# Optimization experiments

Hardware: AMD Instinct MI355X
Metric: run time of the kernel (lower is better)

## Reference

```python
import jax, jax.numpy as jnp
import numpy as np

DIM = 2048
N_HEADS = 16
N_KV_HEADS = 4
HEAD_DIM = 128
EPS = 1e-6
BS, SEQ = 2, 4096


def setup_inputs() -> dict:
    key = jax.random.key(0)
    ks = jax.random.split(key, 8)
    x = jax.random.normal(ks[0], (BS, SEQ, DIM), dtype=jnp.float32)
    # rotary freqs: unit-modulus complex represented as [seq, head_dim//2, 2]
    theta = 10000.0
    inv_freq = 1.0 / (theta ** (jnp.arange(0, HEAD_DIM, 2, dtype=jnp.float32) / HEAD_DIM))
    t = jnp.arange(SEQ, dtype=jnp.float32)
    ang = jnp.outer(t, inv_freq)  # [SEQ, HEAD_DIM//2]
    freqs_cis = jnp.stack([jnp.cos(ang), jnp.sin(ang)], axis=-1)  # [SEQ, HD/2, 2]
    std = 0.02
    wq = jax.random.normal(ks[1], (N_HEADS * HEAD_DIM, DIM), dtype=jnp.float32) * std
    wk = jax.random.normal(ks[2], (N_KV_HEADS * HEAD_DIM, DIM), dtype=jnp.float32) * std
    wv = jax.random.normal(ks[3], (N_KV_HEADS * HEAD_DIM, DIM), dtype=jnp.float32) * std
    wo = jax.random.normal(ks[4], (DIM, N_HEADS * HEAD_DIM), dtype=jnp.float32) * std
    q_norm_w = jnp.ones((HEAD_DIM,), dtype=jnp.float32)
    k_norm_w = jnp.ones((HEAD_DIM,), dtype=jnp.float32)
    return {"x": x, "freqs_cis": freqs_cis, "wq": wq, "wk": wk, "wv": wv,
            "wo": wo, "q_norm_w": q_norm_w, "k_norm_w": k_norm_w}


def _rms_norm(x, w, eps=EPS):
    xf = x.astype(jnp.float32)
    var = jnp.mean(xf * xf, axis=-1, keepdims=True)
    return w * (xf * jax.lax.rsqrt(var + eps)).astype(x.dtype)


def _apply_rope(x, freqs_cis):
    # x: [b, s, h, d]; freqs_cis: [s, d//2, 2] (cos, sin)
    b, s, h, d = x.shape
    xr = x.astype(jnp.float32).reshape(b, s, h, d // 2, 2)
    cos = freqs_cis[:s, :, 0][None, :, None, :]
    sin = freqs_cis[:s, :, 1][None, :, None, :]
    xre, xim = xr[..., 0], xr[..., 1]
    out = jnp.stack([xre * cos - xim * sin, xre * sin + xim * cos], axis=-1)
    return out.reshape(b, s, h, d).astype(x.dtype)


def reference(x, freqs_cis, wq, wk, wv, wo, q_norm_w, k_norm_w):
    bs, seqlen, _ = x.shape
    xq = jnp.einsum('bsd,ed->bse', x, wq).reshape(bs, seqlen, N_HEADS, HEAD_DIM)
    xk = jnp.einsum('bsd,ed->bse', x, wk).reshape(bs, seqlen, N_KV_HEADS, HEAD_DIM)
    xv = jnp.einsum('bsd,ed->bse', x, wv).reshape(bs, seqlen, N_KV_HEADS, HEAD_DIM)
    xq = _rms_norm(xq, q_norm_w)
    xk = _rms_norm(xk, k_norm_w)
    xq = _apply_rope(xq, freqs_cis)
    xk = _apply_rope(xk, freqs_cis)
    n_rep = N_HEADS // N_KV_HEADS
    # repeat_kv: [b,s,kvh,d] -> [b,s,kvh*n_rep,d]
    keys = jnp.repeat(xk, n_rep, axis=2)
    values = jnp.repeat(xv, n_rep, axis=2)
    q = xq.transpose(0, 2, 1, 3)  # [b,h,s,d]
    k = keys.transpose(0, 2, 1, 3)
    v = values.transpose(0, 2, 1, 3)
    scale = 1.0 / jnp.sqrt(jnp.asarray(HEAD_DIM, dtype=q.dtype))
    scores = jnp.einsum('bhqd,bhkd->bhqk', q, k) * scale
    causal = jnp.tril(jnp.ones((seqlen, seqlen), dtype=bool))
    scores = jnp.where(causal[None, None], scores, jnp.finfo(scores.dtype).min)
    attn = jax.nn.softmax(scores, axis=-1)
    out = jnp.einsum('bhqk,bhkd->bhqd', attn, v)
    out = out.transpose(0, 2, 1, 3).reshape(bs, seqlen, N_HEADS * HEAD_DIM)
    return jnp.einsum('bse,de->bsd', out, wo)
```

## Files before the change

kernel.cpp:

```cpp
#include <hip/hip_runtime.h>

typedef __bf16 bf16;
typedef __bf16 bf16x8 __attribute__((ext_vector_type(8)));
typedef __bf16 bf16x4 __attribute__((ext_vector_type(4)));
typedef __bf16 bf16x2 __attribute__((ext_vector_type(2)));
typedef float  f32x4  __attribute__((ext_vector_type(4)));

static_assert(sizeof(bf16x8) == 16, "bf16x8 must be 16B");

#define MFMA16(a, b, c) __builtin_amdgcn_mfma_f32_16x16x32_bf16((a), (b), (c), 0, 0, 0)

__device__ __forceinline__ void gload_lds16(const void* g, void* l) {
    __builtin_amdgcn_global_load_lds(
        (const __attribute__((address_space(1))) void*)(uintptr_t)g,
        (__attribute__((address_space(3))) void*)(uintptr_t)l,
        16, 0, 0);
}

__global__ __launch_bounds__(256)
void cast_f32_bf16(const float* __restrict__ in, bf16* __restrict__ out, int n8)
{
    const int i = blockIdx.x * 256 + threadIdx.x;
    if (i >= n8) return;
    const float4 a = ((const float4*)in)[i * 2];
    const float4 b = ((const float4*)in)[i * 2 + 1];
    bf16x8 o;
    o[0] = (bf16)a.x; o[1] = (bf16)a.y; o[2] = (bf16)a.z; o[3] = (bf16)a.w;
    o[4] = (bf16)b.x; o[5] = (bf16)b.y; o[6] = (bf16)b.z; o[7] = (bf16)b.w;
    ((bf16x8*)out)[i] = o;
}

template <typename OT>
__global__ __launch_bounds__(256)
void gemm_bt(const bf16* __restrict__ A, const bf16* __restrict__ W,
             int K, int ldc, OT* __restrict__ C)
{
    __shared__ bf16 As[128 * 32];
    __shared__ bf16 Bs[128 * 32];

    const int n0 = blockIdx.x * 128;
    const int m0 = blockIdx.y * 128;

    const int tid  = threadIdx.x;
    const int lane = tid & 63;
    const int wid  = tid >> 6;
    const int wm   = wid >> 1;
    const int wn   = wid & 1;
    const int quad = lane >> 4;
    const int l16  = lane & 15;

    const int srow = wid * 32 + (lane >> 2);
    const int scol = (lane & 3) * 8;
    const bf16* ag = A + (size_t)(m0 + srow) * K + scol;
    const bf16* wg = W + (size_t)(n0 + srow) * K + scol;
    bf16* al = As + wid * 1024;
    bf16* bl = Bs + wid * 1024;

    const bf16* afr = As + (wm * 64 + l16) * 32 + quad * 8;
    const bf16* bfr = Bs + (wn * 64 + l16) * 32 + quad * 8;

    f32x4 acc[4][4];
#pragma unroll
    for (int i = 0; i < 4; i++)
#pragma unroll
        for (int j = 0; j < 4; j++) acc[i][j] = f32x4{0.f, 0.f, 0.f, 0.f};

    for (int kt = 0; kt < K; kt += 32) {
        __syncthreads();
        gload_lds16(ag,          al);
        gload_lds16(ag + 16 * K, al + 512);
        gload_lds16(wg,          bl);
        gload_lds16(wg + 16 * K, bl + 512);
        ag += 32; wg += 32;
        __syncthreads();

        bf16x8 af[4], bfv[4];
#pragma unroll
        for (int i = 0; i < 4; i++) af[i]  = *(const bf16x8*)(afr + i * 16 * 32);
#pragma unroll
        for (int i = 0; i < 4; i++) bfv[i] = *(const bf16x8*)(bfr + i * 16 * 32);
#pragma unroll
        for (int mi = 0; mi < 4; mi++)
#pragma unroll
            for (int ni = 0; ni < 4; ni++)
                acc[mi][ni] = MFMA16(af[mi], bfv[ni], acc[mi][ni]);
    }

#pragma unroll
    for (int mi = 0; mi < 4; mi++) {
        const int row = m0 + wm * 64 + mi * 16 + quad * 4;
#pragma unroll
        for (int ni = 0; ni < 4; ni++) {
            const int col = n0 + wn * 64 + ni * 16 + l16;
#pragma unroll
            for (int r = 0; r < 4; r++)
                C[(size_t)(row + r) * ldc + col] = (OT)acc[mi][ni][r];
        }
    }
}

__global__ __launch_bounds__(256)
void normrope(bf16* __restrict__ qkv, const float* __restrict__ fc,
              const float* __restrict__ qw, const float* __restrict__ kw)
{
    const int row  = blockIdx.x * 4 + (threadIdx.x >> 6);
    const int lane = threadIdx.x & 63;
    const int slot = row % 20;
    const int tok  = row / 20;
    const int s    = tok & 4095;

    const float* w; int off; float post;
    if (slot < 16) { off = slot * 128;               w = qw; post = 0.12751681555f; }
    else           { off = 2048 + (slot - 16) * 128; w = kw; post = 1.0f; }

    bf16* p = qkv + (size_t)tok * 3072 + off;

    bf16x2 v = *(const bf16x2*)(p + 2 * lane);
    float x0 = (float)v[0], x1 = (float)v[1];

    float ss = x0 * x0 + x1 * x1;
    ss += __shfl_xor(ss, 1);  ss += __shfl_xor(ss, 2);  ss += __shfl_xor(ss, 4);
    ss += __shfl_xor(ss, 8);  ss += __shfl_xor(ss, 16); ss += __shfl_xor(ss, 32);
    const float r = rsqrtf(ss * (1.0f / 128.0f) + 1e-6f) * post;

    const float xn0 = x0 * r * w[2 * lane], xn1 = x1 * r * w[2 * lane + 1];

    const float2 cs = ((const float2*)fc)[(size_t)s * 64 + lane];
    const float c = cs.x, sn = cs.y;

    bf16x2 o;
    o[0] = (bf16)(xn0 * c - xn1 * sn);
    o[1] = (bf16)(xn0 * sn + xn1 * c);
    *(bf16x2*)(p + 2 * lane) = o;
}

__global__ __launch_bounds__(256)
void transpose_v(const bf16* __restrict__ qkv, bf16* __restrict__ vT)
{
    const int idx = blockIdx.x;
    const int d   = idx & 127;
    const int bk  = idx >> 7;
    const int b   = bk >> 2;
    const int kvh = bk & 3;
    const bf16* src = qkv + (size_t)b * 4096 * 3072 + 2560 + kvh * 128 + d;
    bf16* dst = vT + (size_t)idx * 4096;
    for (int s = threadIdx.x; s < 4096; s += 256)
        dst[s] = src[(size_t)s * 3072];
}

__global__ __launch_bounds__(256)
void flash(const bf16* __restrict__ qkv, const bf16* __restrict__ vT,
           bf16* __restrict__ out)
{
    const int bh  = blockIdx.y;
    const int b   = bh >> 4, h = bh & 15;
    const int kvh = h >> 2;

    const int tid  = threadIdx.x;
    const int lane = tid & 63;
    const int wid  = tid >> 6;
    const int quad = lane >> 4;
    const int l16  = lane & 15;
    const int key  = l16 & 7;

    __shared__ bf16 Ks[2][64 * 128];
    __shared__ bf16 Vs[128 * 64];
    __shared__ bf16 Ps[128 * 64];

    const bf16* kbase = qkv + (size_t)b * 4096 * 3072 + 2048 + kvh * 128;
    const bf16* vbase = vT + ((size_t)(b * 4 + kvh) * 128) * 4096;

    const int krow_off = lane >> 4;
    const int kcolg    = lane & 15;
    const int vrow_off = lane >> 3;
    const int vcolg    = lane & 7;

    for (int pass = 0; pass < 2; ++pass) {
        const int qt = pass ? (31 - blockIdx.x) : blockIdx.x;
        const int q0 = qt * 128;
        const int ntiles = qt * 2 + 2;

        __syncthreads();
#pragma unroll
        for (int i = 0; i < 4; i++) {
            const int r0 = wid * 16 + i * 4;
            const int rk = r0 + krow_off;
            const int gc = (kcolg ^ (rk & 7)) * 8;
            gload_lds16(kbase + (size_t)rk * 3072 + gc, &Ks[0][r0 * 128]);
        }

        bf16x8 qf[2][4];
        const bf16* qbase = qkv + ((size_t)(b * 4096 + q0 + wid * 32)) * 3072 + h * 128;
#pragma unroll
        for (int mt = 0; mt < 2; mt++)
#pragma unroll
            for (int ks = 0; ks < 4; ks++)
                qf[mt][ks] = *(const bf16x8*)(qbase + (size_t)(mt * 16 + l16) * 3072 + ks * 32 + quad * 8);

        f32x4 oacc[2][8];
#pragma unroll
        for (int mt = 0; mt < 2; mt++)
#pragma unroll
            for (int nd = 0; nd < 8; nd++) oacc[mt][nd] = f32x4{0.f, 0.f, 0.f, 0.f};
        float mrow[2], lrow[2];
#pragma unroll
        for (int mt = 0; mt < 2; mt++) { mrow[mt] = -__builtin_inff(); lrow[mt] = 0.f; }

        int cur = 0;
        for (int t = 0; t < ntiles; t++) {
            const int kv0 = t * 64;
            __syncthreads();

#pragma unroll
            for (int i = 0; i < 4; i++) {
                const int r0 = wid * 32 + i * 8;
                const int dv = r0 + vrow_off;
                const int gc = (vcolg ^ (dv & 7)) * 8;
                gload_lds16(vbase + (size_t)dv * 4096 + kv0 + gc, &Vs[r0 * 64]);
            }
            const int kvn = (t + 1 < ntiles) ? kv0 + 64 : kv0;
#pragma unroll
            for (int i = 0; i < 4; i++) {
                const int r0 = wid * 16 + i * 4;
                const int rk = r0 + krow_off;
                const int gc = (kcolg ^ (rk & 7)) * 8;
                gload_lds16(kbase + (size_t)(kvn + rk) * 3072 + gc, &Ks[1 - cur][r0 * 128]);
            }

            f32x4 sacc[2][4];
#pragma unroll
            for (int mt = 0; mt < 2; mt++)
#pragma unroll
                for (int nt = 0; nt < 4; nt++) sacc[mt][nt] = f32x4{0.f, 0.f, 0.f, 0.f};
            __builtin_amdgcn_s_setprio(1);
#pragma unroll
            for (int ks = 0; ks < 4; ks++) {
                bf16x8 kf[4];
#pragma unroll
                for (int nt = 0; nt < 4; nt++)
                    kf[nt] = *(const bf16x8*)(&Ks[cur][(nt * 16 + l16) * 128 + (((ks * 4 + quad) ^ key) * 8)]);
#pragma unroll
                for (int mt = 0; mt < 2; mt++)
#pragma unroll
                    for (int nt = 0; nt < 4; nt++)
                        sacc[mt][nt] = MFMA16(kf[nt], qf[mt][ks], sacc[mt][nt]);
            }
            __builtin_amdgcn_s_setprio(0);

            if (kv0 + 63 > q0) {
#pragma unroll
                for (int mt = 0; mt < 2; mt++) {
                    const int qg = q0 + wid * 32 + mt * 16 + l16;
#pragma unroll
                    for (int nt = 0; nt < 4; nt++)
#pragma unroll
                        for (int r = 0; r < 4; r++) {
                            const int kvg = kv0 + nt * 16 + quad * 4 + r;
                            if (kvg > qg) sacc[mt][nt][r] = -1e30f;
                        }
                }
            }

            float pm[2];
#pragma unroll
            for (int mt = 0; mt < 2; mt++) {
                float t8[8];
#pragma unroll
                for (int nt = 0; nt < 4; nt++) {
                    t8[2 * nt]     = fmaxf(sacc[mt][nt][0], sacc[mt][nt][1]);
                    t8[2 * nt + 1] = fmaxf(sacc[mt][nt][2], sacc[mt][nt][3]);
                }
                float m = fmaxf(fmaxf(fmaxf(t8[0], t8[1]), fmaxf(t8[2], t8[3])),
                                fmaxf(fmaxf(t8[4], t8[5]), fmaxf(t8[6], t8[7])));
                m = fmaxf(m, __shfl_xor(m, 16));
                m = fmaxf(m, __shfl_xor(m, 32));
                pm[mt] = m;
            }

            const bool rescale =
                !__all((pm[0] - mrow[0] <= 8.f) && (pm[1] - mrow[1] <= 8.f));
            if (rescale) {
#pragma unroll
                for (int mt = 0; mt < 2; mt++) {
                    const float mnew  = fmaxf(mrow[mt], pm[mt]);
                    const float alpha = exp2f(mrow[mt] - mnew);
                    mrow[mt] = mnew;
                    lrow[mt] *= alpha;
                    float ar[4];
#pragma unroll
                    for (int r = 0; r < 4; r++) ar[r] = __shfl(alpha, quad * 4 + r);
#pragma unroll
                    for (int nd = 0; nd < 8; nd++)
#pragma unroll
                        for (int r = 0; r < 4; r++) oacc[mt][nd][r] *= ar[r];
                }
            }

#pragma unroll
            for (int mt = 0; mt < 2; mt++) {
                const int prow = wid * 32 + mt * 16 + l16;
                float sn[4];
#pragma unroll
                for (int nt = 0; nt < 4; nt++) {
                    const float p0 = exp2f(sacc[mt][nt][0] - mrow[mt]);
                    const float p1 = exp2f(sacc[mt][nt][1] - mrow[mt]);
                    const float p2 = exp2f(sacc[mt][nt][2] - mrow[mt]);
                    const float p3 = exp2f(sacc[mt][nt][3] - mrow[mt]);
                    sn[nt] = (p0 + p1) + (p2 + p3);
                    bf16x4 h4;
                    h4[0] = (bf16)p0; h4[1] = (bf16)p1;
                    h4[2] = (bf16)p2; h4[3] = (bf16)p3;
                    const int g = (2 * nt + (quad >> 1)) ^ key;
                    *(bf16x4*)(&Ps[prow * 64 + g * 8 + (quad & 1) * 4]) = h4;
                }
                float s = (sn[0] + sn[1]) + (sn[2] + sn[3]);
                s += __shfl_xor(s, 16);
                s += __shfl_xor(s, 32);
                lrow[mt] += s;
            }

            __syncthreads();

            __builtin_amdgcn_s_setprio(1);
#pragma unroll
            for (int ks = 0; ks < 2; ks++) {
                bf16x8 pf[2];
#pragma unroll
                for (int mt = 0; mt < 2; mt++)
                    pf[mt] = *(const bf16x8*)(&Ps[(wid * 32 + mt * 16 + l16) * 64 + (((ks * 4 + quad) ^ key) * 8)]);
#pragma unroll
                for (int nd = 0; nd < 8; nd++) {
                    const bf16x8 vf = *(const bf16x8*)(&Vs[(nd * 16 + l16) * 64 + (((ks * 4 + quad) ^ key) * 8)]);
#pragma unroll
                    for (int mt = 0; mt < 2; mt++)
                        oacc[mt][nd] = MFMA16(pf[mt], vf, oacc[mt][nd]);
                }
            }
            __builtin_amdgcn_s_setprio(0);
            cur ^= 1;
        }

#pragma unroll
        for (int mt = 0; mt < 2; mt++) {
            const float inv = 1.0f / lrow[mt];
            float invr[4];
#pragma unroll
            for (int r = 0; r < 4; r++) invr[r] = __shfl(inv, quad * 4 + r);
#pragma unroll
            for (int r = 0; r < 4; r++) {
                const size_t srow = (size_t)(b * 4096 + q0 + wid * 32 + mt * 16 + quad * 4 + r);
#pragma unroll
                for (int nd = 0; nd < 8; nd++)
                    out[srow * 2048 + h * 128 + nd * 16 + l16] = (bf16)(oacc[mt][nd][r] * invr[r]);
            }
        }
    }
}

extern "C" void kernel_launch(void* const* d_in, const int* in_sizes, int n_in,
                              void* d_out, int out_size, void* d_ws, size_t ws_size,
                              hipStream_t stream)
{
    const float* x   = (const float*)d_in[0];
    const float* fc  = (const float*)d_in[1];
    const float* wq  = (const float*)d_in[2];
    const float* wk  = (const float*)d_in[3];
    const float* wv  = (const float*)d_in[4];
    const float* wo  = (const float*)d_in[5];
    const float* qnw = (const float*)d_in[6];
    const float* knw = (const float*)d_in[7];
    float* out = (float*)d_out;

    char* ws = (char*)d_ws;
    bf16* qkv = (bf16*)ws;
    bf16* vT  = (bf16*)(ws + 50331648);
    bf16* xb  = (bf16*)(ws + 58720256);
    bf16* att = xb;
    bf16* wb  = (bf16*)(ws + 92274688);
    bf16* wob = wb;

    cast_f32_bf16<<<dim3(8192), 256, 0, stream>>>(x, xb, 2097152);
    cast_f32_bf16<<<dim3(2048), 256, 0, stream>>>(wq, wb, 524288);
    cast_f32_bf16<<<dim3(512),  256, 0, stream>>>(wk, wb + 2048 * 2048, 131072);
    cast_f32_bf16<<<dim3(512),  256, 0, stream>>>(wv, wb + 2560 * 2048, 131072);
    gemm_bt<bf16><<<dim3(24, 64), 256, 0, stream>>>(xb, wb, 2048, 3072, qkv);
    normrope<<<dim3(40960), 256, 0, stream>>>(qkv, fc, qnw, knw);
    transpose_v<<<dim3(1024), 256, 0, stream>>>(qkv, vT);
    flash<<<dim3(16, 32), 256, 0, stream>>>(qkv, vT, att);
    cast_f32_bf16<<<dim3(2048), 256, 0, stream>>>(wo, wob, 524288);
    gemm_bt<float><<<dim3(16, 64), 256, 0, stream>>>(att, wob, 2048, 2048, out);
}
```

Before: 696.9 us.

## Compute softmax row sums via MFMA with ones, tile V transpose through LDS

The flash kernel now accumulates the softmax denominator by running an extra MFMA of the bf16 P fragments against a vector of ones. This replaces the per-tile exp-sum adds and cross-lane shuffles, and the sum now uses the bf16-rounded P, which matches the numerator. The V transpose kernel moves from strided scalar loads to 64x128 tiles staged through shared memory, giving coalesced reads and writes. The redundant K prefetch on the last tile is also skipped. The cost is extra MFMA work and slightly different rounding in the normaliser.

```diff
diff --git a/kernel.cpp b/kernel.cpp
--- a/kernel.cpp
+++ b/kernel.cpp
@@ -137,15 +137,32 @@
 __global__ __launch_bounds__(256)
 void transpose_v(const bf16* __restrict__ qkv, bf16* __restrict__ vT)
 {
-    const int idx = blockIdx.x;
-    const int d   = idx & 127;
-    const int bk  = idx >> 7;
-    const int b   = bk >> 2;
-    const int kvh = bk & 3;
-    const bf16* src = qkv + (size_t)b * 4096 * 3072 + 2560 + kvh * 128 + d;
-    bf16* dst = vT + (size_t)idx * 4096;
-    for (int s = threadIdx.x; s < 4096; s += 256)
-        dst[s] = src[(size_t)s * 3072];
+    __shared__ bf16 T[64][130];
+    const int st = blockIdx.x;
+    const int bk = blockIdx.y;
+    const int b = bk >> 2, kvh = bk & 3;
+    const int w = threadIdx.x >> 6, lane = threadIdx.x & 63;
+    const int s0 = st * 64;
+
+    const bf16* src = qkv + (size_t)(b * 4096 + s0) * 3072 + 2560 + kvh * 128;
+#pragma unroll
+    for (int i = 0; i < 16; i++) {
+        const int s = w * 16 + i;
+        const bf16x2 v = *(const bf16x2*)(src + (size_t)s * 3072 + 2 * lane);
+        *(bf16x2*)(&T[s][2 * lane]) = v;
+    }
+    __syncthreads();
+
+    bf16* dst = vT + ((size_t)bk * 128) * 4096 + s0;
+#pragma unroll
+    for (int i = 0; i < 16; i++) {
+        const int d = w * 32 + 2 * i + (lane >> 5);
+        const int s = (lane & 31) * 2;
+        bf16x2 o;
+        o[0] = T[s][d];
+        o[1] = T[s + 1][d];
+        *(bf16x2*)(dst + (size_t)d * 4096 + s) = o;
+    }
 }
 
 __global__ __launch_bounds__(256)
@@ -175,6 +192,10 @@
     const int vrow_off = lane >> 3;
     const int vcolg    = lane & 7;
 
+    bf16x8 vone;
+#pragma unroll
+    for (int j = 0; j < 8; j++) vone[j] = (bf16)1.0f;
+
     for (int pass = 0; pass < 2; ++pass) {
         const int qt = pass ? (31 - blockIdx.x) : blockIdx.x;
         const int q0 = qt * 128;
@@ -198,13 +219,16 @@
                 qf[mt][ks] = *(const bf16x8*)(qbase + (size_t)(mt * 16 + l16) * 3072 + ks * 32 + quad * 8);
 
         f32x4 oacc[2][8];
-#pragma unroll
-        for (int mt = 0; mt < 2; mt++)
+        f32x4 lacc[2];
+#pragma unroll
+        for (int mt = 0; mt < 2; mt++) {
 #pragma unroll
             for (int nd = 0; nd < 8; nd++) oacc[mt][nd] = f32x4{0.f, 0.f, 0.f, 0.f};
-        float mrow[2], lrow[2];
-#pragma unroll
-        for (int mt = 0; mt < 2; mt++) { mrow[mt] = -__builtin_inff(); lrow[mt] = 0.f; }
+            lacc[mt] = f32x4{0.f, 0.f, 0.f, 0.f};
+        }
+        float mrow[2];
+#pragma unroll
+        for (int mt = 0; mt < 2; mt++) mrow[mt] = -__builtin_inff();
 
         int cur = 0;
         for (int t = 0; t < ntiles; t++) {
@@ -218,13 +242,15 @@
                 const int gc = (vcolg ^ (dv & 7)) * 8;
                 gload_lds16(vbase + (size_t)dv * 4096 + kv0 + gc, &Vs[r0 * 64]);
             }
-            const int kvn = (t + 1 < ntiles) ? kv0 + 64 : kv0;
-#pragma unroll
-            for (int i = 0; i < 4; i++) {
-                const int r0 = wid * 16 + i * 4;
-                const int rk = r0 + krow_off;
-                const int gc = (kcolg ^ (rk & 7)) * 8;
-                gload_lds16(kbase + (size_t)(kvn + rk) * 3072 + gc, &Ks[1 - cur][r0 * 128]);
+            if (t + 1 < ntiles) {
+                const int kvn = kv0 + 64;
+#pragma unroll
+                for (int i = 0; i < 4; i++) {
+                    const int r0 = wid * 16 + i * 4;
+                    const int rk = r0 + krow_off;
+                    const int gc = (kcolg ^ (rk & 7)) * 8;
+                    gload_lds16(kbase + (size_t)(kvn + rk) * 3072 + gc, &Ks[1 - cur][r0 * 128]);
+                }
             }
 
             f32x4 sacc[2][4];
@@ -285,7 +311,6 @@
                     const float mnew  = fmaxf(mrow[mt], pm[mt]);
                     const float alpha = exp2f(mrow[mt] - mnew);
                     mrow[mt] = mnew;
-                    lrow[mt] *= alpha;
                     float ar[4];
 #pragma unroll
                     for (int r = 0; r < 4; r++) ar[r] = __shfl(alpha, quad * 4 + r);
@@ -293,30 +318,26 @@
                     for (int nd = 0; nd < 8; nd++)
 #pragma unroll
                         for (int r = 0; r < 4; r++) oacc[mt][nd][r] *= ar[r];
+#pragma unroll
+                    for (int r = 0; r < 4; r++) lacc[mt][r] *= ar[r];
                 }
             }
 
 #pragma unroll
             for (int mt = 0; mt < 2; mt++) {
                 const int prow = wid * 32 + mt * 16 + l16;
-                float sn[4];
 #pragma unroll
                 for (int nt = 0; nt < 4; nt++) {
                     const float p0 = exp2f(sacc[mt][nt][0] - mrow[mt]);
                     const float p1 = exp2f(sacc[mt][nt][1] - mrow[mt]);
                     const float p2 = exp2f(sacc[mt][nt][2] - mrow[mt]);
                     const float p3 = exp2f(sacc[mt][nt][3] - mrow[mt]);
-                    sn[nt] = (p0 + p1) + (p2 + p3);
                     bf16x4 h4;
                     h4[0] = (bf16)p0; h4[1] = (bf16)p1;
                     h4[2] = (bf16)p2; h4[3] = (bf16)p3;
                     const int g = (2 * nt + (quad >> 1)) ^ key;
                     *(bf16x4*)(&Ps[prow * 64 + g * 8 + (quad & 1) * 4]) = h4;
                 }
-                float s = (sn[0] + sn[1]) + (sn[2] + sn[3]);
-                s += __shfl_xor(s, 16);
-                s += __shfl_xor(s, 32);
-                lrow[mt] += s;
             }
 
             __syncthreads();
@@ -335,6 +356,9 @@
                     for (int mt = 0; mt < 2; mt++)
                         oacc[mt][nd] = MFMA16(pf[mt], vf, oacc[mt][nd]);
                 }
+#pragma unroll
+                for (int mt = 0; mt < 2; mt++)
+                    lacc[mt] = MFMA16(pf[mt], vone, lacc[mt]);
             }
             __builtin_amdgcn_s_setprio(0);
             cur ^= 1;
@@ -342,16 +366,13 @@
 
 #pragma unroll
         for (int mt = 0; mt < 2; mt++) {
-            const float inv = 1.0f / lrow[mt];
-            float invr[4];
-#pragma unroll
-            for (int r = 0; r < 4; r++) invr[r] = __shfl(inv, quad * 4 + r);
 #pragma unroll
             for (int r = 0; r < 4; r++) {
+                const float inv = 1.0f / lacc[mt][r];
                 const size_t srow = (size_t)(b * 4096 + q0 + wid * 32 + mt * 16 + quad * 4 + r);
 #pragma unroll
                 for (int nd = 0; nd < 8; nd++)
-                    out[srow * 2048 + h * 128 + nd * 16 + l16] = (bf16)(oacc[mt][nd][r] * invr[r]);
+                    out[srow * 2048 + h * 128 + nd * 16 + l16] = (bf16)(oacc[mt][nd][r] * inv);
             }
         }
     }
@@ -385,7 +406,7 @@
     cast_f32_bf16<<<dim3(512),  256, 0, stream>>>(wv, wb + 2560 * 2048, 131072);
     gemm_bt<bf16><<<dim3(24, 64), 256, 0, stream>>>(xb, wb, 2048, 3072, qkv);
     normrope<<<dim3(40960), 256, 0, stream>>>(qkv, fc, qnw, knw);
-    transpose_v<<<dim3(1024), 256, 0, stream>>>(qkv, vT);
+    transpose_v<<<dim3(64, 8), 256, 0, stream>>>(qkv, vT);
     flash<<<dim3(16, 32), 256, 0, stream>>>(qkv, vT, att);
     cast_f32_bf16<<<dim3(2048), 256, 0, stream>>>(wo, wob, 524288);
     gemm_bt<float><<<dim3(16, 64), 256, 0, stream>>>(att, wob, 2048, 2048, out);
```

New measurement: 686.6 us. About the same (-1.5%).
